# Kernel optimization log

Hardware: AMD Instinct MI355X
Metric: run time of the kernel (lower is better)

The kernel has to match this reference:

```python
import jax, jax.numpy as jnp
import numpy as np

ANCHORS = np.array([116., 90., 156., 198., 373., 326.], np.float32).reshape(1, 1, 1, 3, 2)
IGNORE_THRESH = 0.5
OBJ_SCALE = 5.0
NOOBJ_SCALE = 1.0
XYWH_SCALE = 1.0
CLASS_SCALE = 1.0
GRID_SCALE = 1.0


def setup_inputs() -> dict:
    key = jax.random.key(0)
    k1, k2, k3 = jax.random.split(key, 3)
    B, GH, GW, NET, T, C = 16, 64, 64, 1024, 100, 80
    input_image = jnp.zeros((B, NET, NET, 3), jnp.float32)  # only shape is used
    y_pred = jax.random.normal(k1, (B, GH, GW, 3 * (5 + C)), jnp.float32)
    y_true = jax.random.uniform(k2, (B, GH, GW, 3, 5 + C), jnp.float32)
    true_boxes = jax.random.uniform(k3, (B, 1, 1, 1, T, 4), jnp.float32)
    return {"input_image": input_image, "y_pred": y_pred, "y_true": y_true, "true_boxes": true_boxes}


def reference(input_image, y_pred, y_true, true_boxes):
    B, GH, GW = y_true.shape[:3]
    net_h, net_w = input_image.shape[1], input_image.shape[2]
    dtype = y_pred.dtype
    anchors = jnp.asarray(ANCHORS, dtype)  # [1,1,1,3,2]
    y_pred = y_pred.reshape(B, GH, GW, 3, -1)
    object_mask = y_true[..., 4:5]  # [B,GH,GW,3,1]
    grid_factor = jnp.array([GW, GH], dtype).reshape(1, 1, 1, 1, 2)
    net_factor = jnp.array([net_w, net_h], dtype).reshape(1, 1, 1, 1, 2)
    cx, cy = jnp.meshgrid(jnp.arange(GW, dtype=dtype), jnp.arange(GH, dtype=dtype))
    cell_grid = jnp.stack([cx, cy], -1)[None, :, :, None, :]  # [1,GH,GW,1,2]

    # adjust predictions
    pred_box_xy = cell_grid + jax.nn.sigmoid(y_pred[..., :2])
    pred_box_wh = y_pred[..., 2:4]
    pred_box_conf = jax.nn.sigmoid(y_pred[..., 4:5])
    pred_box_class = y_pred[..., 5:]

    # adjust ground truth
    true_box_xy = y_true[..., 0:2]
    true_box_wh = y_true[..., 2:4]
    true_box_class = jnp.argmax(y_true[..., 5:], axis=-1)  # [B,GH,GW,3]

    # broadcast IoU: each predicted box vs all true boxes
    true_xy = true_boxes[..., 0:2] / grid_factor  # [B,1,1,1,T,2]
    true_wh = true_boxes[..., 2:4] / net_factor
    true_half = true_wh / 2.0
    true_mins, true_maxes = true_xy - true_half, true_xy + true_half
    pred_xy = (pred_box_xy / grid_factor)[..., None, :]  # [B,GH,GW,3,1,2]
    pred_wh = (jnp.exp(pred_box_wh) * anchors / net_factor)[..., None, :]
    pred_half = pred_wh / 2.0
    pred_mins, pred_maxes = pred_xy - pred_half, pred_xy + pred_half
    inter_wh = jnp.maximum(jnp.minimum(pred_maxes, true_maxes) - jnp.maximum(pred_mins, true_mins), 0.0)
    inter_area = inter_wh[..., 0] * inter_wh[..., 1]  # [B,GH,GW,3,T]
    true_area = true_wh[..., 0] * true_wh[..., 1]
    pred_area = pred_wh[..., 0] * pred_wh[..., 1]
    iou = inter_area / (pred_area + true_area - inter_area)
    best_ious = jnp.max(iou, axis=4)
    conf_ignore_mask = (best_ious > IGNORE_THRESH).astype(dtype)[..., None]

    # post-warmup branch (batch_seen > warmup_batches)
    xywh_mask = object_mask

    wh_scale = jnp.exp(true_box_wh) * anchors / net_factor
    wh_scale = (2.0 - wh_scale[..., 0] * wh_scale[..., 1])[..., None]

    xy_delta = xywh_mask * (true_box_xy - pred_box_xy) * wh_scale * XYWH_SCALE
    wh_delta = xywh_mask * (true_box_wh - pred_box_wh) * wh_scale * XYWH_SCALE
    conf_delta = (0.0 - pred_box_conf) * NOOBJ_SCALE
    conf_delta = conf_delta + object_mask * (1.0 - pred_box_conf) * OBJ_SCALE
    conf_delta = conf_delta * (1.0 - (1.0 - object_mask) * conf_ignore_mask)
    log_p = jax.nn.log_softmax(pred_box_class, axis=-1)
    ce = -jnp.take_along_axis(log_p, true_box_class[..., None], axis=-1)  # [B,GH,GW,3,1]
    class_delta = object_mask * ce * CLASS_SCALE

    delta = jnp.concatenate([xy_delta, wh_delta, conf_delta, class_delta], axis=-1)  # [B,GH,GW,3,6]
    loss = jnp.sum(jnp.square(delta), axis=(1, 2, 3, 4))
    return loss * GRID_SCALE
```

## Files before the change

### kernel.cpp

```cpp
#include <hip/hip_runtime.h>


#define GH 64
#define GW 64
#define NA 3
#define NC 80
#define NT 100
#define CPB (GH * GW * NA)
#define NTOT (16 * CPB)

__device__ __forceinline__ float frcp(float x) { return __builtin_amdgcn_rcpf(x); }
__device__ __forceinline__ float fsig(float x) { return frcp(1.f + __expf(-x)); }

__global__ __launch_bounds__(256) void yolo_loss_kernel(
    const float* __restrict__ y_pred,
    const float* __restrict__ y_true,
    const float* __restrict__ true_boxes,
    float* __restrict__ out)
{
    __shared__ float4 sbox[NT];
    __shared__ float  sarea[NT];
    __shared__ float  swsum[4];

    const int tid = threadIdx.x;
    const int idx = blockIdx.x * 256 + tid;
    const int b   = idx / CPB;

    if (tid < NT) {
        const float4 tb = *(const float4*)(true_boxes + (size_t)b * NT * 4 + tid * 4);
        float tx = tb.x * (1.f / GW),     ty = tb.y * (1.f / GH);
        float tw = tb.z * (1.f / 1024.f), th = tb.w * (1.f / 1024.f);
        sbox[tid]  = make_float4(tx - 0.5f * tw, ty - 0.5f * th,
                                 tx + 0.5f * tw, ty + 0.5f * th);
        sarea[tid] = tw * th;
    }
    __syncthreads();

    const int rem = idx % CPB;
    const int gy  = rem / (GW * NA);
    const int r2  = rem - gy * (GW * NA);
    const int gx  = r2 / NA;
    const int a   = r2 - gx * NA;

    const float aw = (a == 0) ? 116.f : ((a == 1) ? 156.f : 373.f);
    const float ah = (a == 0) ? 90.f  : ((a == 1) ? 198.f : 326.f);

    const float* p = y_pred + (size_t)idx * 85;
    const float* t = y_true + (size_t)idx * 85;

    const float p0 = p[0], p1 = p[1], p2 = p[2], p3 = p[3], p4 = p[4];
    const float t0 = t[0], t1 = t[1], t2 = t[2], t3 = t[3], om = t[4];

    float pc[NC];
#pragma unroll
    for (int j = 0; j < NC; ++j) pc[j] = p[5 + j];

    float m = pc[0];
#pragma unroll
    for (int j = 1; j < NC; ++j) m = fmaxf(m, pc[j]);
    float s = 0.f;
#pragma unroll
    for (int j = 0; j < NC; ++j) s += __expf(pc[j] - m);
    const float lse = m + __logf(s);

    float tmax = -1.f, psel = 0.f;
#pragma unroll
    for (int j = 0; j < NC; ++j) {
        const float tj = t[5 + j];
        const bool g = tj > tmax;
        tmax = g ? tj : tmax;
        psel = g ? pc[j] : psel;
    }
    const float ce = lse - psel;

    const float predx = (float)gx + fsig(p0);
    const float predy = (float)gy + fsig(p1);
    const float conf  = fsig(p4);
    const float pw = __expf(p2) * aw * (1.f / 1024.f);
    const float ph = __expf(p3) * ah * (1.f / 1024.f);
    const float parea = pw * ph;
    const float px = predx * (1.f / GW), py = predy * (1.f / GH);
    const float pminx = px - 0.5f * pw, pmaxx = px + 0.5f * pw;
    const float pminy = py - 0.5f * ph, pmaxy = py + 0.5f * ph;

    float best = 0.f;
#pragma unroll 4
    for (int ti = 0; ti < NT; ++ti) {
        const float4 bx = sbox[ti];
        float iw = fminf(pmaxx, bx.z) - fmaxf(pminx, bx.x);
        float ih = fminf(pmaxy, bx.w) - fmaxf(pminy, bx.y);
        iw = fmaxf(iw, 0.f); ih = fmaxf(ih, 0.f);
        const float inter = iw * ih;
        const float iou = inter * frcp(parea + sarea[ti] - inter);
        best = fmaxf(best, iou);
    }
    const float ignore = (best > 0.5f) ? 1.f : 0.f;

    const float wsx = __expf(t2) * aw * (1.f / 1024.f);
    const float wsy = __expf(t3) * ah * (1.f / 1024.f);
    const float ws  = 2.f - wsx * wsy;
    const float omws = om * ws;

    const float dx = omws * (t0 - predx);
    const float dy = omws * (t1 - predy);
    const float dw = omws * (t2 - p2);
    const float dh = omws * (t3 - p3);
    float dc = -conf + om * (1.f - conf) * 5.f;
    dc *= (1.f - (1.f - om) * ignore);
    const float dcl = om * ce;

    float val = dx * dx + dy * dy + dw * dw + dh * dh + dc * dc + dcl * dcl;

#pragma unroll
    for (int off = 32; off > 0; off >>= 1) val += __shfl_down(val, off, 64);
    if ((tid & 63) == 0) swsum[tid >> 6] = val;
    __syncthreads();
    if (tid == 0) atomicAdd(out + b, swsum[0] + swsum[1] + swsum[2] + swsum[3]);
}

extern "C" void kernel_launch(void* const* d_in, const int* in_sizes, int n_in,
                              void* d_out, int out_size, void* d_ws, size_t ws_size,
                              hipStream_t stream) {
    const float* y_pred     = (const float*)d_in[1];
    const float* y_true     = (const float*)d_in[2];
    const float* true_boxes = (const float*)d_in[3];
    float* out = (float*)d_out;

    hipMemsetAsync(d_out, 0, (size_t)out_size * sizeof(float), stream);
    yolo_loss_kernel<<<NTOT / 256, 256, 0, stream>>>(y_pred, y_true, true_boxes, out);
}
```

Baseline: 314.7 us.

## Stage rows through LDS with coalesced float4 loads and split each row across 8 lanes

Each wave now loads 8-row chunks of y_pred and y_true with coalesced float4 reads into per-wave LDS, prefetching the next chunk into registers while the current one is computed. Each row is handled by 8 lanes that split the 80-class softmax, the argmax and the 100-box IoU scan, then combine results with xor shuffles. This replaces strided per-thread loads of 85-float rows and cuts register pressure from holding 80 class logits per thread. It adds shuffle and LDS traffic and redundant per-lane scalar math, and the per-block partial sums now go out as one atomic per wave.

```diff
diff --git a/kernel.cpp b/kernel.cpp
--- a/kernel.cpp
+++ b/kernel.cpp
@@ -1,34 +1,43 @@
 #include <hip/hip_runtime.h>
 
 
-#define GH 64
-#define GW 64
-#define NA 3
 #define NC 80
 #define NT 100
-#define CPB (GH * GW * NA)
-#define NTOT (16 * CPB)
+#define ROW_F 85
+#define CPB 12288
+#define NTOT 196608
+#define ROWS_PER_BLOCK 128
+#define ROWS_PER_WAVE 32
+#define CHUNK_ROWS 8
+#define NCHUNK 4
+#define CHUNK_F 680
+#define CHUNK_F4 170
 
 __device__ __forceinline__ float frcp(float x) { return __builtin_amdgcn_rcpf(x); }
 __device__ __forceinline__ float fsig(float x) { return frcp(1.f + __expf(-x)); }
 
-__global__ __launch_bounds__(256) void yolo_loss_kernel(
+__global__ __launch_bounds__(256, 4) void yolo_loss_kernel(
     const float* __restrict__ y_pred,
     const float* __restrict__ y_true,
     const float* __restrict__ true_boxes,
     float* __restrict__ out)
 {
+    __shared__ __align__(16) float slds[4][2 * CHUNK_F];
     __shared__ float4 sbox[NT];
     __shared__ float  sarea[NT];
-    __shared__ float  swsum[4];
 
-    const int tid = threadIdx.x;
-    const int idx = blockIdx.x * 256 + tid;
-    const int b   = idx / CPB;
+    const int tid  = threadIdx.x;
+    const int widx = tid >> 6;
+    const int lane = tid & 63;
+    const int r    = lane >> 3;
+    const int q    = lane & 7;
+
+    const int block_row0 = blockIdx.x * ROWS_PER_BLOCK;
+    const int b = block_row0 / CPB;
 
     if (tid < NT) {
         const float4 tb = *(const float4*)(true_boxes + (size_t)b * NT * 4 + tid * 4);
-        float tx = tb.x * (1.f / GW),     ty = tb.y * (1.f / GH);
+        float tx = tb.x * (1.f / 64.f),   ty = tb.y * (1.f / 64.f);
         float tw = tb.z * (1.f / 1024.f), th = tb.w * (1.f / 1024.f);
         sbox[tid]  = make_float4(tx - 0.5f * tw, ty - 0.5f * th,
                                  tx + 0.5f * tw, ty + 0.5f * th);
@@ -36,86 +45,116 @@
     }
     __syncthreads();
 
-    const int rem = idx % CPB;
-    const int gy  = rem / (GW * NA);
-    const int r2  = rem - gy * (GW * NA);
-    const int gx  = r2 / NA;
-    const int a   = r2 - gx * NA;
+    const int wave_row0 = block_row0 + widx * ROWS_PER_WAVE;
+    float* S = slds[widx];
 
-    const float aw = (a == 0) ? 116.f : ((a == 1) ? 156.f : 373.f);
-    const float ah = (a == 0) ? 90.f  : ((a == 1) ? 198.f : 326.f);
+    float4 a0, a1, b0, b1;
+    float4 a2 = make_float4(0, 0, 0, 0), b2 = make_float4(0, 0, 0, 0);
+    auto issue = [&](int c) {
+        const size_t off = (size_t)(wave_row0 + c * CHUNK_ROWS) * ROW_F;
+        const float4* gp4 = (const float4*)(y_pred + off);
+        const float4* gt4 = (const float4*)(y_true + off);
+        a0 = gp4[lane]; a1 = gp4[lane + 64];
+        b0 = gt4[lane]; b1 = gt4[lane + 64];
+        if (lane < CHUNK_F4 - 128) { a2 = gp4[lane + 128]; b2 = gt4[lane + 128]; }
+    };
+    issue(0);
 
-    const float* p = y_pred + (size_t)idx * 85;
-    const float* t = y_true + (size_t)idx * 85;
+    float acc = 0.f;
+    for (int c = 0; c < NCHUNK; ++c) {
+        float4* SP = (float4*)S;
+        float4* ST = (float4*)(S + CHUNK_F);
+        SP[lane] = a0; SP[lane + 64] = a1;
+        ST[lane] = b0; ST[lane + 64] = b1;
+        if (lane < CHUNK_F4 - 128) { SP[lane + 128] = a2; ST[lane + 128] = b2; }
 
-    const float p0 = p[0], p1 = p[1], p2 = p[2], p3 = p[3], p4 = p[4];
-    const float t0 = t[0], t1 = t[1], t2 = t[2], t3 = t[3], om = t[4];
+        if (c + 1 < NCHUNK) issue(c + 1);
 
-    float pc[NC];
+        __builtin_amdgcn_s_waitcnt(0xC07F);
+        __builtin_amdgcn_wave_barrier();
+
+        const float* P = S + r * ROW_F;
+        const float* T = P + CHUNK_F;
+        const float p0 = P[0], p1 = P[1], p2 = P[2], p3 = P[3], p4 = P[4];
+        const float t0 = T[0], t1 = T[1], t2 = T[2], t3 = T[3], om = T[4];
+
+        const int grow = wave_row0 + c * CHUNK_ROWS + r;
+        const int rem  = grow - b * CPB;
+        const int gy   = rem / 192;
+        const int rr   = rem - gy * 192;
+        const int gx   = rr / 3;
+        const int a    = rr - gx * 3;
+        const float aw = (a == 0) ? 116.f : ((a == 1) ? 156.f : 373.f);
+        const float ah = (a == 0) ? 90.f  : ((a == 1) ? 198.f : 326.f);
+
+        const int cb = 5 + 10 * q;
+        float mloc = -1e30f;
 #pragma unroll
-    for (int j = 0; j < NC; ++j) pc[j] = p[5 + j];
+        for (int k = 0; k < 10; ++k) mloc = fmaxf(mloc, P[cb + k]);
+        float tmax = -1e30f; int jm = 0;
+#pragma unroll
+        for (int k = 0; k < 10; ++k) {
+            const float tv = T[cb + k];
+            if (tv > tmax) { tmax = tv; jm = cb - 5 + k; }
+        }
+#pragma unroll
+        for (int off = 1; off < 8; off <<= 1) {
+            mloc = fmaxf(mloc, __shfl_xor(mloc, off, 64));
+            const float otv = __shfl_xor(tmax, off, 64);
+            const int   oj  = __shfl_xor(jm, off, 64);
+            if (otv > tmax || (otv == tmax && oj < jm)) { tmax = otv; jm = oj; }
+        }
+        float sl = 0.f;
+#pragma unroll
+        for (int k = 0; k < 10; ++k) sl += __expf(P[cb + k] - mloc);
+#pragma unroll
+        for (int off = 1; off < 8; off <<= 1) sl += __shfl_xor(sl, off, 64);
+        const float lse = mloc + __logf(sl);
+        const float ce  = lse - P[5 + jm];
 
-    float m = pc[0];
+        const float predx = (float)gx + fsig(p0);
+        const float predy = (float)gy + fsig(p1);
+        const float conf  = fsig(p4);
+        const float pw = __expf(p2) * aw * (1.f / 1024.f);
+        const float ph = __expf(p3) * ah * (1.f / 1024.f);
+        const float parea = pw * ph;
+        const float px = predx * (1.f / 64.f), py = predy * (1.f / 64.f);
+        const float pminx = px - 0.5f * pw, pmaxx = px + 0.5f * pw;
+        const float pminy = py - 0.5f * ph, pmaxy = py + 0.5f * ph;
+
+        float best = 0.f;
+        for (int ti = q; ti < NT; ti += 8) {
+            const float4 bx = sbox[ti];
+            float iw = fminf(pmaxx, bx.z) - fmaxf(pminx, bx.x);
+            float ih = fminf(pmaxy, bx.w) - fmaxf(pminy, bx.y);
+            iw = fmaxf(iw, 0.f); ih = fmaxf(ih, 0.f);
+            const float inter = iw * ih;
+            best = fmaxf(best, inter * frcp(parea + sarea[ti] - inter));
+        }
 #pragma unroll
-    for (int j = 1; j < NC; ++j) m = fmaxf(m, pc[j]);
-    float s = 0.f;
-#pragma unroll
-    for (int j = 0; j < NC; ++j) s += __expf(pc[j] - m);
-    const float lse = m + __logf(s);
+        for (int off = 1; off < 8; off <<= 1)
+            best = fmaxf(best, __shfl_xor(best, off, 64));
+        const float ignore = (best > 0.5f) ? 1.f : 0.f;
 
-    float tmax = -1.f, psel = 0.f;
-#pragma unroll
-    for (int j = 0; j < NC; ++j) {
-        const float tj = t[5 + j];
-        const bool g = tj > tmax;
-        tmax = g ? tj : tmax;
-        psel = g ? pc[j] : psel;
+        const float wsx = __expf(t2) * aw * (1.f / 1024.f);
+        const float wsy = __expf(t3) * ah * (1.f / 1024.f);
+        const float ws  = 2.f - wsx * wsy;
+        const float omws = om * ws;
+        const float dx = omws * (t0 - predx);
+        const float dy = omws * (t1 - predy);
+        const float dw = omws * (t2 - p2);
+        const float dh = omws * (t3 - p3);
+        float dc = -conf + om * (1.f - conf) * 5.f;
+        dc *= (1.f - (1.f - om) * ignore);
+        const float dcl = om * ce;
+
+        const float val = dx * dx + dy * dy + dw * dw + dh * dh + dc * dc + dcl * dcl;
+        acc += (q == 0) ? val : 0.f;
     }
-    const float ce = lse - psel;
-
-    const float predx = (float)gx + fsig(p0);
-    const float predy = (float)gy + fsig(p1);
-    const float conf  = fsig(p4);
-    const float pw = __expf(p2) * aw * (1.f / 1024.f);
-    const float ph = __expf(p3) * ah * (1.f / 1024.f);
-    const float parea = pw * ph;
-    const float px = predx * (1.f / GW), py = predy * (1.f / GH);
-    const float pminx = px - 0.5f * pw, pmaxx = px + 0.5f * pw;
-    const float pminy = py - 0.5f * ph, pmaxy = py + 0.5f * ph;
-
-    float best = 0.f;
-#pragma unroll 4
-    for (int ti = 0; ti < NT; ++ti) {
-        const float4 bx = sbox[ti];
-        float iw = fminf(pmaxx, bx.z) - fmaxf(pminx, bx.x);
-        float ih = fminf(pmaxy, bx.w) - fmaxf(pminy, bx.y);
-        iw = fmaxf(iw, 0.f); ih = fmaxf(ih, 0.f);
-        const float inter = iw * ih;
-        const float iou = inter * frcp(parea + sarea[ti] - inter);
-        best = fmaxf(best, iou);
-    }
-    const float ignore = (best > 0.5f) ? 1.f : 0.f;
-
-    const float wsx = __expf(t2) * aw * (1.f / 1024.f);
-    const float wsy = __expf(t3) * ah * (1.f / 1024.f);
-    const float ws  = 2.f - wsx * wsy;
-    const float omws = om * ws;
-
-    const float dx = omws * (t0 - predx);
-    const float dy = omws * (t1 - predy);
-    const float dw = omws * (t2 - p2);
-    const float dh = omws * (t3 - p3);
-    float dc = -conf + om * (1.f - conf) * 5.f;
-    dc *= (1.f - (1.f - om) * ignore);
-    const float dcl = om * ce;
-
-    float val = dx * dx + dy * dy + dw * dw + dh * dh + dc * dc + dcl * dcl;
 
 #pragma unroll
-    for (int off = 32; off > 0; off >>= 1) val += __shfl_down(val, off, 64);
-    if ((tid & 63) == 0) swsum[tid >> 6] = val;
-    __syncthreads();
-    if (tid == 0) atomicAdd(out + b, swsum[0] + swsum[1] + swsum[2] + swsum[3]);
+    for (int off = 32; off > 0; off >>= 1) acc += __shfl_down(acc, off, 64);
+    if (lane == 0) atomicAdd(out + b, acc);
 }
 
 extern "C" void kernel_launch(void* const* d_in, const int* in_sizes, int n_in,
@@ -127,5 +166,5 @@
     float* out = (float*)d_out;
 
     hipMemsetAsync(d_out, 0, (size_t)out_size * sizeof(float), stream);
-    yolo_loss_kernel<<<NTOT / 256, 256, 0, stream>>>(y_pred, y_true, true_boxes, out);
+    yolo_loss_kernel<<<NTOT / ROWS_PER_BLOCK, 256, 0, stream>>>(y_pred, y_true, true_boxes, out);
 }
```

After: 362.6 us. +15.2%, slower.

## Vectorize class loads with software-prefetched batches and drop max-subtraction in softmax

Applied to the files above, without the earlier changes.

Class logits and targets are now read as 4-wide vectors (4-byte aligned) in five batches of 16, with the next batch loaded while the current one is processed. The log-sum-exp no longer subtracts the maximum, which removes a pass over the 80 logits but can overflow for large inputs. The true-box area is recomputed inside the IoU loop instead of being read from a separate shared array, and launch bounds now request 4 blocks per CU. The aim is to cut register pressure and load instruction count, at the cost of numerical robustness and some extra arithmetic in the IoU loop.

```diff
diff --git a/kernel.cpp b/kernel.cpp
--- a/kernel.cpp
+++ b/kernel.cpp
@@ -1,110 +1,123 @@
 #include <hip/hip_runtime.h>
 
 
-#define GH 64
-#define GW 64
-#define NA 3
 #define NC 80
 #define NT 100
-#define CPB (GH * GW * NA)
-#define NTOT (16 * CPB)
+#define CPB 12288
+#define NTOT 196608
+
+typedef float f4 __attribute__((ext_vector_type(4)));
+typedef f4 f4a __attribute__((aligned(4)));
 
 __device__ __forceinline__ float frcp(float x) { return __builtin_amdgcn_rcpf(x); }
 __device__ __forceinline__ float fsig(float x) { return frcp(1.f + __expf(-x)); }
 
-__global__ __launch_bounds__(256) void yolo_loss_kernel(
+__global__ __launch_bounds__(256, 4) void yolo_loss_kernel(
     const float* __restrict__ y_pred,
     const float* __restrict__ y_true,
     const float* __restrict__ true_boxes,
     float* __restrict__ out)
 {
-    __shared__ float4 sbox[NT];
-    __shared__ float  sarea[NT];
-    __shared__ float  swsum[4];
+    __shared__ f4 sbox[NT];
+    __shared__ float swsum[4];
 
     const int tid = threadIdx.x;
     const int idx = blockIdx.x * 256 + tid;
     const int b   = idx / CPB;
 
     if (tid < NT) {
-        const float4 tb = *(const float4*)(true_boxes + (size_t)b * NT * 4 + tid * 4);
-        float tx = tb.x * (1.f / GW),     ty = tb.y * (1.f / GH);
-        float tw = tb.z * (1.f / 1024.f), th = tb.w * (1.f / 1024.f);
-        sbox[tid]  = make_float4(tx - 0.5f * tw, ty - 0.5f * th,
-                                 tx + 0.5f * tw, ty + 0.5f * th);
-        sarea[tid] = tw * th;
+        const f4 tb = *(const f4*)(true_boxes + (size_t)b * NT * 4 + tid * 4);
+        const float tx = tb.x * (1.f / 64.f),   ty = tb.y * (1.f / 64.f);
+        const float tw = tb.z * (1.f / 1024.f), th = tb.w * (1.f / 1024.f);
+        f4 r;
+        r.x = tx - 0.5f * tw; r.y = ty - 0.5f * th;
+        r.z = tx + 0.5f * tw; r.w = ty + 0.5f * th;
+        sbox[tid] = r;
     }
     __syncthreads();
 
     const int rem = idx % CPB;
-    const int gy  = rem / (GW * NA);
-    const int r2  = rem - gy * (GW * NA);
-    const int gx  = r2 / NA;
-    const int a   = r2 - gx * NA;
-
+    const int gy  = rem / 192;
+    const int rr  = rem - gy * 192;
+    const int gx  = rr / 3;
+    const int a   = rr - gx * 3;
     const float aw = (a == 0) ? 116.f : ((a == 1) ? 156.f : 373.f);
     const float ah = (a == 0) ? 90.f  : ((a == 1) ? 198.f : 326.f);
 
     const float* p = y_pred + (size_t)idx * 85;
     const float* t = y_true + (size_t)idx * 85;
 
-    const float p0 = p[0], p1 = p[1], p2 = p[2], p3 = p[3], p4 = p[4];
-    const float t0 = t[0], t1 = t[1], t2 = t[2], t3 = t[3], om = t[4];
+    const f4 ph = *(const f4a*)p;   const float p4v = p[4];
+    const f4 th = *(const f4a*)t;   const float om  = t[4];
 
-    float pc[NC];
+    const f4a* pc4 = (const f4a*)(p + 5);
+    const f4a* tc4 = (const f4a*)(t + 5);
+
+    float ssum = 0.f;
+    float tmax = -1e30f, psel = 0.f;
+
+    f4 pa[4], ta[4];
 #pragma unroll
-    for (int j = 0; j < NC; ++j) pc[j] = p[5 + j];
+    for (int k = 0; k < 4; ++k) { pa[k] = pc4[k]; ta[k] = tc4[k]; }
 
-    float m = pc[0];
 #pragma unroll
-    for (int j = 1; j < NC; ++j) m = fmaxf(m, pc[j]);
-    float s = 0.f;
+    for (int bch = 0; bch < 5; ++bch) {
+        f4 pb[4], tb[4];
 #pragma unroll
-    for (int j = 0; j < NC; ++j) s += __expf(pc[j] - m);
-    const float lse = m + __logf(s);
+        for (int k = 0; k < 4; ++k) { pb[k] = pa[k]; tb[k] = ta[k]; }
+        if (bch < 4) {
+#pragma unroll
+            for (int k = 0; k < 4; ++k) {
+                pa[k] = pc4[(bch + 1) * 4 + k];
+                ta[k] = tc4[(bch + 1) * 4 + k];
+            }
+        }
+#pragma unroll
+        for (int k = 0; k < 4; ++k) {
+#pragma unroll
+            for (int c = 0; c < 4; ++c) {
+                const float pv = pb[k][c];
+                const float tv = tb[k][c];
+                ssum += __expf(pv);
+                const bool g = tv > tmax;
+                tmax = g ? tv : tmax;
+                psel = g ? pv : psel;
+            }
+        }
+    }
+    const float ce = __logf(ssum) - psel;
 
-    float tmax = -1.f, psel = 0.f;
-#pragma unroll
-    for (int j = 0; j < NC; ++j) {
-        const float tj = t[5 + j];
-        const bool g = tj > tmax;
-        tmax = g ? tj : tmax;
-        psel = g ? pc[j] : psel;
-    }
-    const float ce = lse - psel;
-
-    const float predx = (float)gx + fsig(p0);
-    const float predy = (float)gy + fsig(p1);
-    const float conf  = fsig(p4);
-    const float pw = __expf(p2) * aw * (1.f / 1024.f);
-    const float ph = __expf(p3) * ah * (1.f / 1024.f);
-    const float parea = pw * ph;
-    const float px = predx * (1.f / GW), py = predy * (1.f / GH);
-    const float pminx = px - 0.5f * pw, pmaxx = px + 0.5f * pw;
-    const float pminy = py - 0.5f * ph, pmaxy = py + 0.5f * ph;
+    const float predx = (float)gx + fsig(ph.x);
+    const float predy = (float)gy + fsig(ph.y);
+    const float conf  = fsig(p4v);
+    const float pw = __expf(ph.z) * aw * (1.f / 1024.f);
+    const float phh = __expf(ph.w) * ah * (1.f / 1024.f);
+    const float parea = pw * phh;
+    const float px = predx * (1.f / 64.f), py = predy * (1.f / 64.f);
+    const float pminx = px - 0.5f * pw,  pmaxx = px + 0.5f * pw;
+    const float pminy = py - 0.5f * phh, pmaxy = py + 0.5f * phh;
 
     float best = 0.f;
 #pragma unroll 4
     for (int ti = 0; ti < NT; ++ti) {
-        const float4 bx = sbox[ti];
+        const f4 bx = sbox[ti];
         float iw = fminf(pmaxx, bx.z) - fmaxf(pminx, bx.x);
         float ih = fminf(pmaxy, bx.w) - fmaxf(pminy, bx.y);
         iw = fmaxf(iw, 0.f); ih = fmaxf(ih, 0.f);
         const float inter = iw * ih;
-        const float iou = inter * frcp(parea + sarea[ti] - inter);
-        best = fmaxf(best, iou);
+        const float tarea = (bx.z - bx.x) * (bx.w - bx.y);
+        best = fmaxf(best, inter * frcp(parea + tarea - inter));
     }
     const float ignore = (best > 0.5f) ? 1.f : 0.f;
 
-    const float wsx = __expf(t2) * aw * (1.f / 1024.f);
-    const float wsy = __expf(t3) * ah * (1.f / 1024.f);
+    const float wsx = __expf(th.z) * aw * (1.f / 1024.f);
+    const float wsy = __expf(th.w) * ah * (1.f / 1024.f);
     const float ws  = 2.f - wsx * wsy;
     const float omws = om * ws;
-
-    const float dx = omws * (t0 - predx);
-    const float dy = omws * (t1 - predy);
-    const float dw = omws * (t2 - p2);
-    const float dh = omws * (t3 - p3);
+    const float dx = omws * (th.x - predx);
+    const float dy = omws * (th.y - predy);
+    const float dw = omws * (th.z - ph.z);
+    const float dh = omws * (th.w - ph.w);
     float dc = -conf + om * (1.f - conf) * 5.f;
     dc *= (1.f - (1.f - om) * ignore);
     const float dcl = om * ce;
```

Result: slower. 366.4 us (+16.4%).
